# Optimization experiments

Hardware: AMD Instinct MI355X
Metric: run time of the kernel (lower is better)

The kernel has to match this reference:

```python
import jax, jax.numpy as jnp
import numpy as np

B, N0, N1, N2 = 4, 50000, 25000, 12500
E0, E1 = 800000, 400000
CIN, CS, COUT = 32, 16, 32
EPS = 1e-5


def _xavier(k, shape):
    scale = (2.0 / (shape[0] + shape[-1])) ** 0.5
    return jax.random.normal(k, shape, jnp.float32) * scale


def setup_inputs() -> dict:
    key = jax.random.key(0)
    ks = jax.random.split(key, 32)
    inp = {
        "X": jax.random.normal(ks[0], (B, N0, CIN), jnp.float32),
        "edge_index0": jax.random.randint(ks[1], (2, E0), 0, N1),
        "edge_weight0": jax.random.uniform(ks[2], (E0,), jnp.float32),
        "res_n_id0": jax.random.randint(ks[3], (N1,), 0, N0),
        "edge_index1": jax.random.randint(ks[4], (2, E1), 0, N2),
        "edge_weight1": jax.random.uniform(ks[5], (E1,), jnp.float32),
        "res_n_id1": jax.random.randint(ks[6], (N2,), 0, N1),
        # conv1 params (in=32 -> out=16, edge_channels=1)
        "Wn1": _xavier(ks[7], (CIN, CS)),
        "We1": _xavier(ks[8], (1, CS)),
        "Q1": _xavier(ks[9], (CS, CS)),
        "K1": _xavier(ks[10], (CS, CS)),
        "Watt1": _xavier(ks[11], (3 * CS, 1)),
        "batt1": jnp.zeros((1,), jnp.float32),
        "Wc1": _xavier(ks[12], (2 * CS, CS)),
        "bc1": jnp.zeros((CS,), jnp.float32),
        # conv2 params (in=16 -> out=32, edge_channels=1)
        "Wn2": _xavier(ks[13], (CS, COUT)),
        "We2": _xavier(ks[14], (1, COUT)),
        "Q2": _xavier(ks[15], (COUT, COUT)),
        "K2": _xavier(ks[16], (COUT, COUT)),
        "Watt2": _xavier(ks[17], (3 * COUT, 1)),
        "batt2": jnp.zeros((1,), jnp.float32),
        "Wc2": _xavier(ks[18], (2 * COUT, COUT)),
        "bc2": jnp.zeros((COUT,), jnp.float32),
    }
    return inp


def egnn_conv(x_src, x_dst, edge_index, edge_feature, num_dst,
              Wn, We, Q, K, Watt, batt, Wc, bc):
    # x_src: [B, Nsrc, Cin], x_dst: [B, Ndst, Cin], edge_feature: [E, 1]
    xs = jnp.matmul(x_src, Wn)        # [B, Nsrc, C]
    xd = jnp.matmul(x_dst, Wn)        # [B, Ndst, C]
    edge_emb = jnp.matmul(edge_feature, We)  # [E, C]

    src, dst = edge_index[0], edge_index[1]
    x_j = xs[:, src]                  # gather [B, E, C]
    x_i = xd[:, dst]                  # gather [B, E, C]

    query = jnp.matmul(x_j, Q)        # [B, E, C]
    key = jnp.matmul(x_i, K)          # [B, E, C]
    ee = jnp.broadcast_to(edge_emb[None], query.shape)  # [B, E, C]
    att_feature = jnp.concatenate([query, key, ee], axis=-1)  # [B, E, 3C]
    att = jax.nn.sigmoid(jnp.matmul(att_feature, Watt) + batt)  # [B, E, 1]
    gate = jax.nn.sigmoid(edge_emb)[None]  # [1, E, C]
    msg = att * x_j * gate            # [B, E, C]

    # scatter-add over destination nodes
    aggr = jnp.zeros((msg.shape[0], num_dst, msg.shape[-1]), msg.dtype)
    aggr = aggr.at[:, dst].add(msg)   # [B, Ndst, C]

    out = jnp.matmul(jnp.concatenate([xd, aggr], axis=-1), Wc) + bc  # [B, Ndst, C]
    mean = jnp.mean(out, axis=(0, 2), keepdims=True)
    var = jnp.var(out, axis=(0, 2), keepdims=True, ddof=1)  # torch var is unbiased
    out = (out - mean) / jnp.sqrt(var + EPS)
    return xd + out


def reference(X, edge_index0, edge_weight0, res_n_id0,
              edge_index1, edge_weight1, res_n_id1,
              Wn1, We1, Q1, K1, Watt1, batt1, Wc1, bc1,
              Wn2, We2, Q2, K2, Watt2, batt2, Wc2, bc2):
    h = egnn_conv(X, X[:, res_n_id0], edge_index0, edge_weight0[:, None], N1,
                  Wn1, We1, Q1, K1, Watt1, batt1, Wc1, bc1)
    h = jax.nn.leaky_relu(h, 0.01)
    h = egnn_conv(h, h[:, res_n_id1], edge_index1, edge_weight1[:, None], N2,
                  Wn2, We2, Q2, K2, Watt2, batt2, Wc2, bc2)
    h = jax.nn.leaky_relu(h, 0.01)
    return h
```

## Files before the change

### kernel.cpp

```cpp
#include <hip/hip_runtime.h>

#define B_ 4
#define N0_ 50000
#define N1_ 25000
#define N2_ 12500
#define E0_ 800000
#define E1_ 400000
#define CIN_ 32
#define CS_ 16
#define COUT_ 32
#define EPS_ 1e-5f
#define CAP_ 80
#define ROW_ CAP_
#define RCAP0_ 14336
#define RCAP1_ 8192
#define NREP_ 8
#define CPAD_ 16
#define SPLITB_ 512
#define SST1_ 3200
#define SST2_ 1600

__device__ __forceinline__ int slice_of(int d) { return (d >> 2) & 7; }
__device__ __forceinline__ int curix(int d, int sst) {
    return ((d >> 2) & 7) * sst + ((d >> 5) << 2) + (d & 3);
}

__device__ __forceinline__ float sigmoidf_(float x) {
    return __builtin_amdgcn_rcpf(1.0f + __expf(-x));
}

__global__ void prep_kernel(const float* __restrict__ Q1, const float* __restrict__ K1,
                            const float* __restrict__ Watt1,
                            const float* __restrict__ Q2, const float* __restrict__ K2,
                            const float* __restrict__ Watt2,
                            const float* __restrict__ We1, const float* __restrict__ We2,
                            float* __restrict__ qv1, float* __restrict__ kv1,
                            float* __restrict__ qv2, float* __restrict__ kv2,
                            float* __restrict__ se) {
    int t = threadIdx.x;
    if (t < CS_) {
        float q = 0.f, k = 0.f;
        for (int c = 0; c < CS_; ++c) {
            q += Q1[t * CS_ + c] * Watt1[c];
            k += K1[t * CS_ + c] * Watt1[CS_ + c];
        }
        qv1[t] = q; kv1[t] = k;
    }
    if (t < COUT_) {
        float q = 0.f, k = 0.f;
        for (int c = 0; c < COUT_; ++c) {
            q += Q2[t * COUT_ + c] * Watt2[c];
            k += K2[t * COUT_ + c] * Watt2[COUT_ + c];
        }
        qv2[t] = q; kv2[t] = k;
    }
    if (t == 0) {
        float s1 = 0.f, s2 = 0.f;
        for (int c = 0; c < CS_; ++c) s1 += We1[c] * Watt1[2 * CS_ + c];
        for (int c = 0; c < COUT_; ++c) s2 += We2[c] * Watt2[2 * COUT_ + c];
        se[0] = s1; se[1] = s2;
    }
}

template <int RCAP>
__device__ __forceinline__ void split_dev(const int* __restrict__ ei, const float* __restrict__ ew,
                                          int E, int* __restrict__ rcnt,
                                          unsigned* __restrict__ A, unsigned short* __restrict__ C,
                                          int bid, int nblocks) {
    __shared__ int lcnt[8];
    __shared__ int lbase[8];
    int tid = threadIdx.x;
    int lane = tid & 63;
    int rep = bid & (NREP_ - 1);
    int per = (E + nblocks - 1) / nblocks;
    int s0 = bid * per;
    int s1 = min(E, s0 + per);
    int niter = (s1 - s0 + 255) >> 8;
    if (tid < 8) lcnt[tid] = 0;
    __syncthreads();
    for (int i = 0; i < niter; ++i) {
        int e = s0 + i * 256 + tid;
        int slice = (e < s1) ? slice_of(ei[E + e]) : -1;
#pragma unroll
        for (int sl = 0; sl < 8; ++sl) {
            unsigned long long m = __ballot(slice == sl);
            if (m && lane == __ffsll(m) - 1) atomicAdd(&lcnt[sl], (int)__popcll(m));
        }
    }
    __syncthreads();
    if (tid < 8) {
        lbase[tid] = atomicAdd(&rcnt[(tid * NREP_ + rep) * CPAD_], lcnt[tid]);
        lcnt[tid] = 0;
    }
    __syncthreads();
    for (int i = 0; i < niter; ++i) {
        int e = s0 + i * 256 + tid;
        int d = 0, s = 0, slice = -1;
        float w = 0.f;
        if (e < s1) {
            d = ei[E + e];
            s = ei[e];
            w = ew[e];
            slice = slice_of(d);
        }
        int pos = 0;
#pragma unroll
        for (int sl = 0; sl < 8; ++sl) {
            unsigned long long m = __ballot(slice == sl);
            if (!m) continue;
            int leader = __ffsll(m) - 1;
            int base = 0;
            if (lane == leader) base = atomicAdd(&lcnt[sl], (int)__popcll(m));
            base = __shfl(base, leader);
            if (slice == sl) pos = base + (int)__popcll(m & ((1ull << lane) - 1ull));
        }
        if (slice >= 0) {
            int gpos = lbase[slice] + pos;
            if (gpos < RCAP) {
                int idx = (slice * NREP_ + rep) * RCAP + gpos;
                A[idx] = (unsigned)d | ((unsigned)s << 16);
                C[idx] = (unsigned short)((__float_as_uint(w) + 0x8000u) >> 16);
            }
        }
    }
}

__global__ void split_both(const int* __restrict__ ei0, const float* __restrict__ ew0,
                           const int* __restrict__ ei1, const float* __restrict__ ew1,
                           int* __restrict__ rcnt0, int* __restrict__ rcnt1,
                           unsigned* __restrict__ A0, unsigned short* __restrict__ C0,
                           unsigned* __restrict__ A1, unsigned short* __restrict__ C1) {
    if (blockIdx.x < SPLITB_)
        split_dev<RCAP0_>(ei0, ew0, E0_, rcnt0, A0, C0, blockIdx.x, SPLITB_);
    else
        split_dev<RCAP1_>(ei1, ew1, E1_, rcnt1, A1, C1, blockIdx.x - SPLITB_, SPLITB_);
}

__global__ void scatter_bin(const int* __restrict__ rcnt0, const unsigned* __restrict__ A0,
                            const unsigned short* __restrict__ C0,
                            int* __restrict__ cur0, unsigned* __restrict__ buf0,
                            const int* __restrict__ rcnt1, const unsigned* __restrict__ A1,
                            const unsigned short* __restrict__ C1,
                            int* __restrict__ cur1b, unsigned* __restrict__ buf1) {
    int half = blockIdx.x >= 1024;
    int bid = blockIdx.x & 1023;
    int slice = bid & 7;
    int chunk = bid >> 3;
    const int nch = 128;
    int tid = threadIdx.x;
    const int* rc = half ? rcnt1 : rcnt0;
    const unsigned* A = half ? A1 : A0;
    const unsigned short* C = half ? C1 : C0;
    int* cur = half ? cur1b : cur0;
    unsigned* buf = half ? buf1 : buf0;
    int RCAP = half ? RCAP1_ : RCAP0_;
    int sst = half ? SST2_ : SST1_;
#pragma unroll
    for (int rep = 0; rep < NREP_; ++rep) {
        int cnt = rc[(slice * NREP_ + rep) * CPAD_];
        if (cnt > RCAP) cnt = RCAP;
        int base = (slice * NREP_ + rep) * RCAP;
        for (int i = chunk * 256 + tid; i < cnt; i += nch * 256) {
            unsigned a = A[base + i];
            int d = a & 0xffff;
            unsigned s = a >> 16;
            unsigned wu = (unsigned)C[base + i];
            int p = atomicAdd(&cur[curix(d, sst)], 1);
            if (p < CAP_)
                buf[(size_t)d * ROW_ + p] = (wu << 16) | s;
        }
    }
}

__global__ void node_xform1(const float* __restrict__ X, const int* __restrict__ res,
                            const float* __restrict__ Wn,
                            const float* __restrict__ qv, const float* __restrict__ kv,
                            unsigned short* __restrict__ xsb, float* __restrict__ xd_t,
                            float* __restrict__ aj, float* __restrict__ ai) {
    int lane = threadIdx.x & 63;
    int n = blockIdx.x * (blockDim.x >> 6) + (threadIdx.x >> 6);
    if (n >= N1_) return;
    int b = lane >> 4;
    int c = lane & 15;
    int rn = res[n];
    const float4* Xs4 = (const float4*)(X + ((size_t)b * N0_ + n) * CIN_);
    const float4* Xd4 = (const float4*)(X + ((size_t)b * N0_ + rn) * CIN_);
    float s = 0.f, d = 0.f;
#pragma unroll
    for (int k4 = 0; k4 < CIN_ / 4; ++k4) {
        float4 xs4 = Xs4[k4];
        float4 xd4 = Xd4[k4];
        int k = 4 * k4;
        float w0 = Wn[(k + 0) * CS_ + c], w1 = Wn[(k + 1) * CS_ + c];
        float w2 = Wn[(k + 2) * CS_ + c], w3 = Wn[(k + 3) * CS_ + c];
        s += xs4.x * w0 + xs4.y * w1 + xs4.z * w2 + xs4.w * w3;
        d += xd4.x * w0 + xd4.y * w1 + xd4.z * w2 + xd4.w * w3;
    }
    xsb[(size_t)n * 64 + lane] = (unsigned short)((__float_as_uint(s) + 0x8000u) >> 16);
    xd_t[(size_t)n * 64 + lane] = d;
    float p = s * qv[c];
    float q = d * kv[c];
#pragma unroll
    for (int m = 1; m < 16; m <<= 1) {
        p += __shfl_xor(p, m, 16);
        q += __shfl_xor(q, m, 16);
    }
    if (c == 0) {
        aj[n * 4 + b] = p;
        ai[n * 4 + b] = q;
    }
}

__global__ void edge_fused1(const int* __restrict__ cur, const unsigned* __restrict__ buf,
                            const unsigned short* __restrict__ xsb,
                            const float* __restrict__ xd_t,
                            const float* __restrict__ aj, const float* __restrict__ ai,
                            const float* __restrict__ sep, const float* __restrict__ batt,
                            const float* __restrict__ We,
                            const float* __restrict__ Wc, const float* __restrict__ bc,
                            float* __restrict__ h_t) {
    int lane = threadIdx.x & 63;
    int n = blockIdx.x * (blockDim.x >> 6) + (threadIdx.x >> 6);
    if (n >= N1_) return;
    int b = lane >> 4;
    int c = lane & 15;
    float wec = We[c];
    float se1 = sep[0];
    float aivb = ai[n * 4 + b] + batt[0];
    float acc = 0.f;
    int cnt = cur[curix(n, SST1_)];
    if (cnt > CAP_) cnt = CAP_;
    const unsigned* bp = buf + (size_t)n * ROW_;
    int i = 0;
    for (; i + 4 <= cnt; i += 4) {
        unsigned v0 = bp[i], v1 = bp[i + 1], v2 = bp[i + 2], v3 = bp[i + 3];
        int s0 = v0 & 0xffff, s1 = v1 & 0xffff, s2 = v2 & 0xffff, s3 = v3 & 0xffff;
        float w0 = __uint_as_float(v0 & 0xffff0000u);
        float w1 = __uint_as_float(v1 & 0xffff0000u);
        float w2 = __uint_as_float(v2 & 0xffff0000u);
        float w3 = __uint_as_float(v3 & 0xffff0000u);
        float aj0 = aj[s0 * 4 + b], aj1 = aj[s1 * 4 + b];
        float aj2 = aj[s2 * 4 + b], aj3 = aj[s3 * 4 + b];
        float xj0 = __uint_as_float((unsigned)xsb[(size_t)s0 * 64 + lane] << 16);
        float xj1 = __uint_as_float((unsigned)xsb[(size_t)s1 * 64 + lane] << 16);
        float xj2 = __uint_as_float((unsigned)xsb[(size_t)s2 * 64 + lane] << 16);
        float xj3 = __uint_as_float((unsigned)xsb[(size_t)s3 * 64 + lane] << 16);
        acc += sigmoidf_(aj0 + aivb + w0 * se1) * sigmoidf_(w0 * wec) * xj0;
        acc += sigmoidf_(aj1 + aivb + w1 * se1) * sigmoidf_(w1 * wec) * xj1;
        acc += sigmoidf_(aj2 + aivb + w2 * se1) * sigmoidf_(w2 * wec) * xj2;
        acc += sigmoidf_(aj3 + aivb + w3 * se1) * sigmoidf_(w3 * wec) * xj3;
    }
    for (; i < cnt; ++i) {
        unsigned v0 = bp[i];
        int s0 = v0 & 0xffff;
        float w0 = __uint_as_float(v0 & 0xffff0000u);
        float aj0 = aj[s0 * 4 + b];
        float xj0 = __uint_as_float((unsigned)xsb[(size_t)s0 * 64 + lane] << 16);
        acc += sigmoidf_(aj0 + aivb + w0 * se1) * sigmoidf_(w0 * wec) * xj0;
    }
    float xv = xd_t[(size_t)n * 64 + lane];
    float o = bc[c];
#pragma unroll
    for (int k = 0; k < CS_; ++k) {
        o += __shfl(xv, k, 16) * Wc[k * CS_ + c];
        o += __shfl(acc, k, 16) * Wc[(CS_ + k) * CS_ + c];
    }
    float s = o, sq = o * o;
#pragma unroll
    for (int m = 1; m < 64; m <<= 1) {
        s += __shfl_xor(s, m);
        sq += __shfl_xor(sq, m);
    }
    float mean = s * (1.f / 64.f);
    float var = (sq - 64.f * mean * mean) * (1.f / 63.f);
    float inv = __builtin_amdgcn_rsqf(var + EPS_);
    float v = xv + (o - mean) * inv;
    h_t[(size_t)n * 64 + lane] = v > 0.f ? v : 0.01f * v;
}

__global__ void node_xform2(const float* __restrict__ h_t, const int* __restrict__ res,
                            const float* __restrict__ Wn,
                            const float* __restrict__ qv, const float* __restrict__ kv,
                            unsigned short* __restrict__ xsb, float* __restrict__ xd_t,
                            float* __restrict__ aj, float* __restrict__ ai) {
    int lane = threadIdx.x & 63;
    int n = blockIdx.x * (blockDim.x >> 6) + (threadIdx.x >> 6);
    if (n >= N2_) return;
    int bl = lane >> 5;
    int c = lane & 31;
    int rn = res[n];
    float qc = qv[c], kc = kv[c];
#pragma unroll
    for (int j = 0; j < 2; ++j) {
        int b = bl + 2 * j;
        const float* hs = h_t + (size_t)n * 64 + b * 16;
        const float* hd = h_t + (size_t)rn * 64 + b * 16;
        float s = 0.f, d = 0.f;
#pragma unroll
        for (int k = 0; k < CS_; ++k) {
            float w = Wn[k * COUT_ + c];
            s += hs[k] * w;
            d += hd[k] * w;
        }
        xsb[(size_t)n * 128 + b * 32 + c] = (unsigned short)((__float_as_uint(s) + 0x8000u) >> 16);
        xd_t[(size_t)n * 128 + b * 32 + c] = d;
        float p = s * qc;
        float q = d * kc;
#pragma unroll
        for (int m = 1; m < 32; m <<= 1) {
            p += __shfl_xor(p, m, 32);
            q += __shfl_xor(q, m, 32);
        }
        if (c == 0) {
            aj[n * 4 + b] = p;
            ai[n * 4 + b] = q;
        }
    }
}

__global__ void edge_fused2(const int* __restrict__ cur, const unsigned* __restrict__ buf,
                            const unsigned short* __restrict__ xsb,
                            const float* __restrict__ xd_t,
                            const float* __restrict__ aj, const float* __restrict__ ai,
                            const float* __restrict__ sep, const float* __restrict__ batt,
                            const float* __restrict__ We,
                            const float* __restrict__ Wc, const float* __restrict__ bc,
                            float* __restrict__ out) {
    int lane = threadIdx.x & 63;
    int n = blockIdx.x * (blockDim.x >> 6) + (threadIdx.x >> 6);
    if (n >= N2_) return;
    int bl = lane >> 5;
    int c = lane & 31;
    float wec = We[c];
    float se2 = sep[0];
    float b0 = batt[0];
    float aiv0 = ai[n * 4 + bl] + b0;
    float aiv1 = ai[n * 4 + bl + 2] + b0;
    float acc0 = 0.f, acc1 = 0.f;
    int cnt = cur[curix(n, SST2_)];
    if (cnt > CAP_) cnt = CAP_;
    const unsigned* bp = buf + (size_t)n * ROW_;
    int i = 0;
    for (; i + 2 <= cnt; i += 2) {
        unsigned v0 = bp[i], v1 = bp[i + 1];
        int s0 = v0 & 0xffff, s1 = v1 & 0xffff;
        float w0 = __uint_as_float(v0 & 0xffff0000u);
        float w1 = __uint_as_float(v1 & 0xffff0000u);
        float aj00 = aj[s0 * 4 + bl], aj01 = aj[s0 * 4 + bl + 2];
        float aj10 = aj[s1 * 4 + bl], aj11 = aj[s1 * 4 + bl + 2];
        float xj00 = __uint_as_float((unsigned)xsb[(size_t)s0 * 128 + lane] << 16);
        float xj01 = __uint_as_float((unsigned)xsb[(size_t)s0 * 128 + 64 + lane] << 16);
        float xj10 = __uint_as_float((unsigned)xsb[(size_t)s1 * 128 + lane] << 16);
        float xj11 = __uint_as_float((unsigned)xsb[(size_t)s1 * 128 + 64 + lane] << 16);
        float g0 = sigmoidf_(w0 * wec);
        float g1 = sigmoidf_(w1 * wec);
        float t0 = w0 * se2, t1 = w1 * se2;
        acc0 += sigmoidf_(aj00 + aiv0 + t0) * g0 * xj00;
        acc1 += sigmoidf_(aj01 + aiv1 + t0) * g0 * xj01;
        acc0 += sigmoidf_(aj10 + aiv0 + t1) * g1 * xj10;
        acc1 += sigmoidf_(aj11 + aiv1 + t1) * g1 * xj11;
    }
    if (i < cnt) {
        unsigned v0 = bp[i];
        int s0 = v0 & 0xffff;
        float w0 = __uint_as_float(v0 & 0xffff0000u);
        float aj00 = aj[s0 * 4 + bl], aj01 = aj[s0 * 4 + bl + 2];
        float xj00 = __uint_as_float((unsigned)xsb[(size_t)s0 * 128 + lane] << 16);
        float xj01 = __uint_as_float((unsigned)xsb[(size_t)s0 * 128 + 64 + lane] << 16);
        float g0 = sigmoidf_(w0 * wec);
        float t0 = w0 * se2;
        acc0 += sigmoidf_(aj00 + aiv0 + t0) * g0 * xj00;
        acc1 += sigmoidf_(aj01 + aiv1 + t0) * g0 * xj01;
    }
    float xv0 = xd_t[(size_t)n * 128 + lane];
    float xv1 = xd_t[(size_t)n * 128 + 64 + lane];
    float o0 = bc[c], o1 = o0;
#pragma unroll
    for (int k = 0; k < COUT_; ++k) {
        float w1 = Wc[k * COUT_ + c];
        float w2 = Wc[(COUT_ + k) * COUT_ + c];
        o0 += __shfl(xv0, k, 32) * w1 + __shfl(acc0, k, 32) * w2;
        o1 += __shfl(xv1, k, 32) * w1 + __shfl(acc1, k, 32) * w2;
    }
    float s = o0 + o1, sq = o0 * o0 + o1 * o1;
#pragma unroll
    for (int m = 1; m < 64; m <<= 1) {
        s += __shfl_xor(s, m);
        sq += __shfl_xor(sq, m);
    }
    float mean = s * (1.f / 128.f);
    float var = (sq - 128.f * mean * mean) * (1.f / 127.f);
    float inv = __builtin_amdgcn_rsqf(var + EPS_);
    float v0 = xv0 + (o0 - mean) * inv;
    float v1 = xv1 + (o1 - mean) * inv;
    out[((size_t)bl * N2_ + n) * COUT_ + c] = v0 > 0.f ? v0 : 0.01f * v0;
    out[((size_t)(bl + 2) * N2_ + n) * COUT_ + c] = v1 > 0.f ? v1 : 0.01f * v1;
}

extern "C" void kernel_launch(void* const* d_in, const int* in_sizes, int n_in,
                              void* d_out, int out_size, void* d_ws, size_t ws_size,
                              hipStream_t stream) {
    (void)in_sizes; (void)n_in; (void)out_size; (void)ws_size;
    const float* X     = (const float*)d_in[0];
    const int*   ei0   = (const int*)d_in[1];
    const float* ew0   = (const float*)d_in[2];
    const int*   rn0   = (const int*)d_in[3];
    const int*   ei1   = (const int*)d_in[4];
    const float* ew1   = (const float*)d_in[5];
    const int*   rn1   = (const int*)d_in[6];
    const float* Wn1   = (const float*)d_in[7];
    const float* We1   = (const float*)d_in[8];
    const float* Q1    = (const float*)d_in[9];
    const float* K1    = (const float*)d_in[10];
    const float* Watt1 = (const float*)d_in[11];
    const float* batt1 = (const float*)d_in[12];
    const float* Wc1   = (const float*)d_in[13];
    const float* bc1   = (const float*)d_in[14];
    const float* Wn2   = (const float*)d_in[15];
    const float* We2   = (const float*)d_in[16];
    const float* Q2    = (const float*)d_in[17];
    const float* K2    = (const float*)d_in[18];
    const float* Watt2 = (const float*)d_in[19];
    const float* batt2 = (const float*)d_in[20];
    const float* Wc2   = (const float*)d_in[21];
    const float* bc2   = (const float*)d_in[22];

    const size_t BUF = (size_t)B_ * N1_ * CS_;
    float* ws  = (float*)d_ws;
    float* S0  = ws;
    float* S1  = S0 + BUF;
    unsigned short* S2 = (unsigned short*)(S1 + BUF);
    float* aj1 = (float*)(S2 + BUF);
    float* ai1 = aj1 + (size_t)N1_ * 4;
    float* aj2 = ai1 + (size_t)N1_ * 4;
    float* ai2 = aj2 + (size_t)N2_ * 4;
    unsigned* ebuf1 = (unsigned*)(ai2 + (size_t)N2_ * 4);
    unsigned* ebuf2 = ebuf1 + (size_t)N1_ * ROW_;
    int* cur1  = (int*)(ebuf2 + (size_t)N2_ * ROW_);
    int* cur2  = cur1 + 8 * SST1_;
    int* rcnt0 = cur2 + 8 * SST2_;
    int* rcnt1 = rcnt0 + 64 * CPAD_;
    unsigned* A0 = (unsigned*)(rcnt1 + 64 * CPAD_);
    unsigned* A1 = A0 + (size_t)64 * RCAP0_;
    unsigned short* C0 = (unsigned short*)(A1 + (size_t)64 * RCAP1_);
    unsigned short* C1 = C0 + (size_t)64 * RCAP0_;
    float* qv1 = (float*)(C1 + (size_t)64 * RCAP1_);
    float* kv1 = qv1 + 16;
    float* qv2 = kv1 + 16;
    float* kv2 = qv2 + 32;
    float* se  = kv2 + 32;

    hipMemsetAsync(cur1, 0, (size_t)(8 * SST1_ + 8 * SST2_ + 128 * CPAD_) * sizeof(int), stream);
    prep_kernel<<<1, 64, 0, stream>>>(Q1, K1, Watt1, Q2, K2, Watt2, We1, We2,
                                      qv1, kv1, qv2, kv2, se);
    split_both<<<2 * SPLITB_, 256, 0, stream>>>(ei0, ew0, ei1, ew1, rcnt0, rcnt1,
                                                A0, C0, A1, C1);
    scatter_bin<<<2048, 256, 0, stream>>>(rcnt0, A0, C0, cur1, ebuf1,
                                          rcnt1, A1, C1, cur2, ebuf2);

    node_xform1<<<(N1_ + 3) / 4, 256, 0, stream>>>(X, rn0, Wn1, qv1, kv1, S2, S0, aj1, ai1);
    edge_fused1<<<(N1_ + 3) / 4, 256, 0, stream>>>(cur1, ebuf1, S2, S0, aj1, ai1,
                                                   se, batt1, We1, Wc1, bc1, S0);

    node_xform2<<<(N2_ + 3) / 4, 256, 0, stream>>>(S0, rn1, Wn2, qv2, kv2, S2, S1, aj2, ai2);
    edge_fused2<<<(N2_ + 3) / 4, 256, 0, stream>>>(cur2, ebuf2, S2, S1, aj2, ai2,
                                                   se + 1, batt2, We2, Wc2, bc2, (float*)d_out);
}
```

Measured before the change: 203.0 us.

## Merge prep/split and bin/xform launches; split edge loops across two waves per node

```diff
diff --git a/kernel.cpp b/kernel.cpp
--- a/kernel.cpp
+++ b/kernel.cpp
@@ -19,47 +19,14 @@
 #define SPLITB_ 512
 #define SST1_ 3200
 #define SST2_ 1600
+#define BINB_ 2048
 
 __device__ __forceinline__ int slice_of(int d) { return (d >> 2) & 7; }
 __device__ __forceinline__ int curix(int d, int sst) {
     return ((d >> 2) & 7) * sst + ((d >> 5) << 2) + (d & 3);
 }
-
 __device__ __forceinline__ float sigmoidf_(float x) {
     return __builtin_amdgcn_rcpf(1.0f + __expf(-x));
-}
-
-__global__ void prep_kernel(const float* __restrict__ Q1, const float* __restrict__ K1,
-                            const float* __restrict__ Watt1,
-                            const float* __restrict__ Q2, const float* __restrict__ K2,
-                            const float* __restrict__ Watt2,
-                            const float* __restrict__ We1, const float* __restrict__ We2,
-                            float* __restrict__ qv1, float* __restrict__ kv1,
-                            float* __restrict__ qv2, float* __restrict__ kv2,
-                            float* __restrict__ se) {
-    int t = threadIdx.x;
-    if (t < CS_) {
-        float q = 0.f, k = 0.f;
-        for (int c = 0; c < CS_; ++c) {
-            q += Q1[t * CS_ + c] * Watt1[c];
-            k += K1[t * CS_ + c] * Watt1[CS_ + c];
-        }
-        qv1[t] = q; kv1[t] = k;
-    }
-    if (t < COUT_) {
-        float q = 0.f, k = 0.f;
-        for (int c = 0; c < COUT_; ++c) {
-            q += Q2[t * COUT_ + c] * Watt2[c];
-            k += K2[t * COUT_ + c] * Watt2[COUT_ + c];
-        }
-        qv2[t] = q; kv2[t] = k;
-    }
-    if (t == 0) {
-        float s1 = 0.f, s2 = 0.f;
-        for (int c = 0; c < CS_; ++c) s1 += We1[c] * Watt1[2 * CS_ + c];
-        for (int c = 0; c < COUT_; ++c) s2 += We2[c] * Watt2[2 * COUT_ + c];
-        se[0] = s1; se[1] = s2;
-    }
 }
 
 template <int RCAP>
@@ -125,103 +92,139 @@
     }
 }
 
-__global__ void split_both(const int* __restrict__ ei0, const float* __restrict__ ew0,
+__global__ void split_prep(const int* __restrict__ ei0, const float* __restrict__ ew0,
                            const int* __restrict__ ei1, const float* __restrict__ ew1,
                            int* __restrict__ rcnt0, int* __restrict__ rcnt1,
                            unsigned* __restrict__ A0, unsigned short* __restrict__ C0,
-                           unsigned* __restrict__ A1, unsigned short* __restrict__ C1) {
-    if (blockIdx.x < SPLITB_)
+                           unsigned* __restrict__ A1, unsigned short* __restrict__ C1,
+                           const float* __restrict__ Q1, const float* __restrict__ K1,
+                           const float* __restrict__ Watt1,
+                           const float* __restrict__ Q2, const float* __restrict__ K2,
+                           const float* __restrict__ Watt2,
+                           const float* __restrict__ We1, const float* __restrict__ We2,
+                           float* __restrict__ qv1, float* __restrict__ kv1,
+                           float* __restrict__ qv2, float* __restrict__ kv2,
+                           float* __restrict__ se) {
+    if (blockIdx.x < SPLITB_) {
         split_dev<RCAP0_>(ei0, ew0, E0_, rcnt0, A0, C0, blockIdx.x, SPLITB_);
-    else
+    } else if (blockIdx.x < 2 * SPLITB_) {
         split_dev<RCAP1_>(ei1, ew1, E1_, rcnt1, A1, C1, blockIdx.x - SPLITB_, SPLITB_);
-}
-
-__global__ void scatter_bin(const int* __restrict__ rcnt0, const unsigned* __restrict__ A0,
-                            const unsigned short* __restrict__ C0,
-                            int* __restrict__ cur0, unsigned* __restrict__ buf0,
-                            const int* __restrict__ rcnt1, const unsigned* __restrict__ A1,
-                            const unsigned short* __restrict__ C1,
-                            int* __restrict__ cur1b, unsigned* __restrict__ buf1) {
-    int half = blockIdx.x >= 1024;
-    int bid = blockIdx.x & 1023;
-    int slice = bid & 7;
-    int chunk = bid >> 3;
-    const int nch = 128;
+    } else {
+        int t = threadIdx.x;
+        if (t < CS_) {
+            float q = 0.f, k = 0.f;
+            for (int c = 0; c < CS_; ++c) {
+                q += Q1[t * CS_ + c] * Watt1[c];
+                k += K1[t * CS_ + c] * Watt1[CS_ + c];
+            }
+            qv1[t] = q; kv1[t] = k;
+        }
+        if (t < COUT_) {
+            float q = 0.f, k = 0.f;
+            for (int c = 0; c < COUT_; ++c) {
+                q += Q2[t * COUT_ + c] * Watt2[c];
+                k += K2[t * COUT_ + c] * Watt2[COUT_ + c];
+            }
+            qv2[t] = q; kv2[t] = k;
+        }
+        if (t == 0) {
+            float s1 = 0.f, s2 = 0.f;
+            for (int c = 0; c < CS_; ++c) s1 += We1[c] * Watt1[2 * CS_ + c];
+            for (int c = 0; c < COUT_; ++c) s2 += We2[c] * Watt2[2 * COUT_ + c];
+            se[0] = s1; se[1] = s2;
+        }
+    }
+}
+
+__global__ void bin_xform1(const int* __restrict__ rcnt0, const unsigned* __restrict__ A0,
+                           const unsigned short* __restrict__ C0,
+                           int* __restrict__ cur0, unsigned* __restrict__ buf0,
+                           const int* __restrict__ rcnt1, const unsigned* __restrict__ A1,
+                           const unsigned short* __restrict__ C1,
+                           int* __restrict__ cur1b, unsigned* __restrict__ buf1,
+                           const float* __restrict__ X, const int* __restrict__ res,
+                           const float* __restrict__ Wn,
+                           const float* __restrict__ qv, const float* __restrict__ kv,
+                           unsigned short* __restrict__ xsb, float* __restrict__ xd_t,
+                           float* __restrict__ aj, float* __restrict__ ai) {
+    if (blockIdx.x < BINB_) {
+        int half = blockIdx.x >= (BINB_ / 2);
+        int bid = blockIdx.x & (BINB_ / 2 - 1);
+        int slice = bid & 7;
+        int chunk = bid >> 3;
+        const int nch = BINB_ / 16;
+        int tid = threadIdx.x;
+        const int* rc = half ? rcnt1 : rcnt0;
+        const unsigned* A = half ? A1 : A0;
+        const unsigned short* C = half ? C1 : C0;
+        int* cur = half ? cur1b : cur0;
+        unsigned* buf = half ? buf1 : buf0;
+        int RCAP = half ? RCAP1_ : RCAP0_;
+        int sst = half ? SST2_ : SST1_;
+#pragma unroll
+        for (int rep = 0; rep < NREP_; ++rep) {
+            int cnt = rc[(slice * NREP_ + rep) * CPAD_];
+            if (cnt > RCAP) cnt = RCAP;
+            int base = (slice * NREP_ + rep) * RCAP;
+            for (int i = chunk * 256 + tid; i < cnt; i += nch * 256) {
+                unsigned a = A[base + i];
+                int d = a & 0xffff;
+                unsigned s = a >> 16;
+                unsigned wu = (unsigned)C[base + i];
+                int p = atomicAdd(&cur[curix(d, sst)], 1);
+                if (p < CAP_)
+                    buf[(size_t)d * ROW_ + p] = (wu << 16) | s;
+            }
+        }
+    } else {
+        int lane = threadIdx.x & 63;
+        int n = (blockIdx.x - BINB_) * 4 + (threadIdx.x >> 6);
+        if (n >= N1_) return;
+        int b = lane >> 4;
+        int c = lane & 15;
+        int rn = res[n];
+        const float4* Xs4 = (const float4*)(X + ((size_t)b * N0_ + n) * CIN_);
+        const float4* Xd4 = (const float4*)(X + ((size_t)b * N0_ + rn) * CIN_);
+        float s = 0.f, d = 0.f;
+#pragma unroll
+        for (int k4 = 0; k4 < CIN_ / 4; ++k4) {
+            float4 xs4 = Xs4[k4];
+            float4 xd4 = Xd4[k4];
+            int k = 4 * k4;
+            float w0 = Wn[(k + 0) * CS_ + c], w1 = Wn[(k + 1) * CS_ + c];
+            float w2 = Wn[(k + 2) * CS_ + c], w3 = Wn[(k + 3) * CS_ + c];
+            s += xs4.x * w0 + xs4.y * w1 + xs4.z * w2 + xs4.w * w3;
+            d += xd4.x * w0 + xd4.y * w1 + xd4.z * w2 + xd4.w * w3;
+        }
+        xsb[(size_t)n * 64 + lane] = (unsigned short)((__float_as_uint(s) + 0x8000u) >> 16);
+        xd_t[(size_t)n * 64 + lane] = d;
+        float p = s * qv[c];
+        float q = d * kv[c];
+#pragma unroll
+        for (int m = 1; m < 16; m <<= 1) {
+            p += __shfl_xor(p, m, 16);
+            q += __shfl_xor(q, m, 16);
+        }
+        if (c == 0) {
+            aj[n * 4 + b] = p;
+            ai[n * 4 + b] = q;
+        }
+    }
+}
+
+__global__ __launch_bounds__(512) void edge_fused1(
+        const int* __restrict__ cur, const unsigned* __restrict__ buf,
+        const unsigned short* __restrict__ xsb, const float* __restrict__ xd_t,
+        const float* __restrict__ aj, const float* __restrict__ ai,
+        const float* __restrict__ sep, const float* __restrict__ batt,
+        const float* __restrict__ We, const float* __restrict__ Wc,
+        const float* __restrict__ bc, float* __restrict__ h_t) {
+    __shared__ float lacc[4][64];
     int tid = threadIdx.x;
-    const int* rc = half ? rcnt1 : rcnt0;
-    const unsigned* A = half ? A1 : A0;
-    const unsigned short* C = half ? C1 : C0;
-    int* cur = half ? cur1b : cur0;
-    unsigned* buf = half ? buf1 : buf0;
-    int RCAP = half ? RCAP1_ : RCAP0_;
-    int sst = half ? SST2_ : SST1_;
-#pragma unroll
-    for (int rep = 0; rep < NREP_; ++rep) {
-        int cnt = rc[(slice * NREP_ + rep) * CPAD_];
-        if (cnt > RCAP) cnt = RCAP;
-        int base = (slice * NREP_ + rep) * RCAP;
-        for (int i = chunk * 256 + tid; i < cnt; i += nch * 256) {
-            unsigned a = A[base + i];
-            int d = a & 0xffff;
-            unsigned s = a >> 16;
-            unsigned wu = (unsigned)C[base + i];
-            int p = atomicAdd(&cur[curix(d, sst)], 1);
-            if (p < CAP_)
-                buf[(size_t)d * ROW_ + p] = (wu << 16) | s;
-        }
-    }
-}
-
-__global__ void node_xform1(const float* __restrict__ X, const int* __restrict__ res,
-                            const float* __restrict__ Wn,
-                            const float* __restrict__ qv, const float* __restrict__ kv,
-                            unsigned short* __restrict__ xsb, float* __restrict__ xd_t,
-                            float* __restrict__ aj, float* __restrict__ ai) {
-    int lane = threadIdx.x & 63;
-    int n = blockIdx.x * (blockDim.x >> 6) + (threadIdx.x >> 6);
-    if (n >= N1_) return;
-    int b = lane >> 4;
-    int c = lane & 15;
-    int rn = res[n];
-    const float4* Xs4 = (const float4*)(X + ((size_t)b * N0_ + n) * CIN_);
-    const float4* Xd4 = (const float4*)(X + ((size_t)b * N0_ + rn) * CIN_);
-    float s = 0.f, d = 0.f;
-#pragma unroll
-    for (int k4 = 0; k4 < CIN_ / 4; ++k4) {
-        float4 xs4 = Xs4[k4];
-        float4 xd4 = Xd4[k4];
-        int k = 4 * k4;
-        float w0 = Wn[(k + 0) * CS_ + c], w1 = Wn[(k + 1) * CS_ + c];
-        float w2 = Wn[(k + 2) * CS_ + c], w3 = Wn[(k + 3) * CS_ + c];
-        s += xs4.x * w0 + xs4.y * w1 + xs4.z * w2 + xs4.w * w3;
-        d += xd4.x * w0 + xd4.y * w1 + xd4.z * w2 + xd4.w * w3;
-    }
-    xsb[(size_t)n * 64 + lane] = (unsigned short)((__float_as_uint(s) + 0x8000u) >> 16);
-    xd_t[(size_t)n * 64 + lane] = d;
-    float p = s * qv[c];
-    float q = d * kv[c];
-#pragma unroll
-    for (int m = 1; m < 16; m <<= 1) {
-        p += __shfl_xor(p, m, 16);
-        q += __shfl_xor(q, m, 16);
-    }
-    if (c == 0) {
-        aj[n * 4 + b] = p;
-        ai[n * 4 + b] = q;
-    }
-}
-
-__global__ void edge_fused1(const int* __restrict__ cur, const unsigned* __restrict__ buf,
-                            const unsigned short* __restrict__ xsb,
-                            const float* __restrict__ xd_t,
-                            const float* __restrict__ aj, const float* __restrict__ ai,
-                            const float* __restrict__ sep, const float* __restrict__ batt,
-                            const float* __restrict__ We,
-                            const float* __restrict__ Wc, const float* __restrict__ bc,
-                            float* __restrict__ h_t) {
-    int lane = threadIdx.x & 63;
-    int n = blockIdx.x * (blockDim.x >> 6) + (threadIdx.x >> 6);
-    if (n >= N1_) return;
+    int lane = tid & 63;
+    int wid = (tid >> 6) & 1;
+    int ni = tid >> 7;
+    int n = blockIdx.x * 4 + ni;
     int b = lane >> 4;
     int c = lane & 15;
     float wec = We[c];
@@ -231,33 +234,39 @@
     int cnt = cur[curix(n, SST1_)];
     if (cnt > CAP_) cnt = CAP_;
     const unsigned* bp = buf + (size_t)n * ROW_;
-    int i = 0;
-    for (; i + 4 <= cnt; i += 4) {
-        unsigned v0 = bp[i], v1 = bp[i + 1], v2 = bp[i + 2], v3 = bp[i + 3];
-        int s0 = v0 & 0xffff, s1 = v1 & 0xffff, s2 = v2 & 0xffff, s3 = v3 & 0xffff;
-        float w0 = __uint_as_float(v0 & 0xffff0000u);
-        float w1 = __uint_as_float(v1 & 0xffff0000u);
-        float w2 = __uint_as_float(v2 & 0xffff0000u);
-        float w3 = __uint_as_float(v3 & 0xffff0000u);
-        float aj0 = aj[s0 * 4 + b], aj1 = aj[s1 * 4 + b];
-        float aj2 = aj[s2 * 4 + b], aj3 = aj[s3 * 4 + b];
-        float xj0 = __uint_as_float((unsigned)xsb[(size_t)s0 * 64 + lane] << 16);
-        float xj1 = __uint_as_float((unsigned)xsb[(size_t)s1 * 64 + lane] << 16);
-        float xj2 = __uint_as_float((unsigned)xsb[(size_t)s2 * 64 + lane] << 16);
-        float xj3 = __uint_as_float((unsigned)xsb[(size_t)s3 * 64 + lane] << 16);
-        acc += sigmoidf_(aj0 + aivb + w0 * se1) * sigmoidf_(w0 * wec) * xj0;
-        acc += sigmoidf_(aj1 + aivb + w1 * se1) * sigmoidf_(w1 * wec) * xj1;
-        acc += sigmoidf_(aj2 + aivb + w2 * se1) * sigmoidf_(w2 * wec) * xj2;
-        acc += sigmoidf_(aj3 + aivb + w3 * se1) * sigmoidf_(w3 * wec) * xj3;
-    }
-    for (; i < cnt; ++i) {
-        unsigned v0 = bp[i];
-        int s0 = v0 & 0xffff;
-        float w0 = __uint_as_float(v0 & 0xffff0000u);
-        float aj0 = aj[s0 * 4 + b];
-        float xj0 = __uint_as_float((unsigned)xsb[(size_t)s0 * 64 + lane] << 16);
-        acc += sigmoidf_(aj0 + aivb + w0 * se1) * sigmoidf_(w0 * wec) * xj0;
-    }
+    for (int i0 = wid * 4; i0 < cnt; i0 += 8) {
+        if (i0 + 4 <= cnt) {
+            uint4 v = *(const uint4*)(bp + i0);
+            int s0 = v.x & 0xffff, s1 = v.y & 0xffff, s2 = v.z & 0xffff, s3 = v.w & 0xffff;
+            float w0 = __uint_as_float(v.x & 0xffff0000u);
+            float w1 = __uint_as_float(v.y & 0xffff0000u);
+            float w2 = __uint_as_float(v.z & 0xffff0000u);
+            float w3 = __uint_as_float(v.w & 0xffff0000u);
+            float aj0 = aj[s0 * 4 + b], aj1 = aj[s1 * 4 + b];
+            float aj2 = aj[s2 * 4 + b], aj3 = aj[s3 * 4 + b];
+            float xj0 = __uint_as_float((unsigned)xsb[(size_t)s0 * 64 + lane] << 16);
+            float xj1 = __uint_as_float((unsigned)xsb[(size_t)s1 * 64 + lane] << 16);
+            float xj2 = __uint_as_float((unsigned)xsb[(size_t)s2 * 64 + lane] << 16);
+            float xj3 = __uint_as_float((unsigned)xsb[(size_t)s3 * 64 + lane] << 16);
+            acc += sigmoidf_(aj0 + aivb + w0 * se1) * sigmoidf_(w0 * wec) * xj0;
+            acc += sigmoidf_(aj1 + aivb + w1 * se1) * sigmoidf_(w1 * wec) * xj1;
+            acc += sigmoidf_(aj2 + aivb + w2 * se1) * sigmoidf_(w2 * wec) * xj2;
+            acc += sigmoidf_(aj3 + aivb + w3 * se1) * sigmoidf_(w3 * wec) * xj3;
+        } else {
+            for (int i = i0; i < cnt; ++i) {
+                unsigned v0 = bp[i];
+                int s0 = v0 & 0xffff;
+                float w0 = __uint_as_float(v0 & 0xffff0000u);
+                float aj0 = aj[s0 * 4 + b];
+                float xj0 = __uint_as_float((unsigned)xsb[(size_t)s0 * 64 + lane] << 16);
+                acc += sigmoidf_(aj0 + aivb + w0 * se1) * sigmoidf_(w0 * wec) * xj0;
+            }
+        }
+    }
+    if (wid == 1) lacc[ni][lane] = acc;
+    __syncthreads();
+    if (wid == 1) return;
+    acc += lacc[ni][lane];
     float xv = xd_t[(size_t)n * 64 + lane];
     float o = bc[c];
 #pragma unroll
@@ -318,17 +327,19 @@
     }
 }
 
-__global__ void edge_fused2(const int* __restrict__ cur, const unsigned* __restrict__ buf,
-                            const unsigned short* __restrict__ xsb,
-                            const float* __restrict__ xd_t,
-                            const float* __restrict__ aj, const float* __restrict__ ai,
-                            const float* __restrict__ sep, const float* __restrict__ batt,
-                            const float* __restrict__ We,
-                            const float* __restrict__ Wc, const float* __restrict__ bc,
-                            float* __restrict__ out) {
-    int lane = threadIdx.x & 63;
-    int n = blockIdx.x * (blockDim.x >> 6) + (threadIdx.x >> 6);
-    if (n >= N2_) return;
+__global__ __launch_bounds__(512) void edge_fused2(
+        const int* __restrict__ cur, const unsigned* __restrict__ buf,
+        const unsigned short* __restrict__ xsb, const float* __restrict__ xd_t,
+        const float* __restrict__ aj, const float* __restrict__ ai,
+        const float* __restrict__ sep, const float* __restrict__ batt,
+        const float* __restrict__ We, const float* __restrict__ Wc,
+        const float* __restrict__ bc, float* __restrict__ out) {
+    __shared__ float lacc[4][2][64];
+    int tid = threadIdx.x;
+    int lane = tid & 63;
+    int wid = (tid >> 6) & 1;
+    int ni = tid >> 7;
+    int n = blockIdx.x * 4 + ni;
     int bl = lane >> 5;
     int c = lane & 31;
     float wec = We[c];
@@ -340,38 +351,45 @@
     int cnt = cur[curix(n, SST2_)];
     if (cnt > CAP_) cnt = CAP_;
     const unsigned* bp = buf + (size_t)n * ROW_;
-    int i = 0;
-    for (; i + 2 <= cnt; i += 2) {
-        unsigned v0 = bp[i], v1 = bp[i + 1];
-        int s0 = v0 & 0xffff, s1 = v1 & 0xffff;
-        float w0 = __uint_as_float(v0 & 0xffff0000u);
-        float w1 = __uint_as_float(v1 & 0xffff0000u);
-        float aj00 = aj[s0 * 4 + bl], aj01 = aj[s0 * 4 + bl + 2];
-        float aj10 = aj[s1 * 4 + bl], aj11 = aj[s1 * 4 + bl + 2];
-        float xj00 = __uint_as_float((unsigned)xsb[(size_t)s0 * 128 + lane] << 16);
-        float xj01 = __uint_as_float((unsigned)xsb[(size_t)s0 * 128 + 64 + lane] << 16);
-        float xj10 = __uint_as_float((unsigned)xsb[(size_t)s1 * 128 + lane] << 16);
-        float xj11 = __uint_as_float((unsigned)xsb[(size_t)s1 * 128 + 64 + lane] << 16);
-        float g0 = sigmoidf_(w0 * wec);
-        float g1 = sigmoidf_(w1 * wec);
-        float t0 = w0 * se2, t1 = w1 * se2;
-        acc0 += sigmoidf_(aj00 + aiv0 + t0) * g0 * xj00;
-        acc1 += sigmoidf_(aj01 + aiv1 + t0) * g0 * xj01;
-        acc0 += sigmoidf_(aj10 + aiv0 + t1) * g1 * xj10;
-        acc1 += sigmoidf_(aj11 + aiv1 + t1) * g1 * xj11;
-    }
-    if (i < cnt) {
-        unsigned v0 = bp[i];
-        int s0 = v0 & 0xffff;
-        float w0 = __uint_as_float(v0 & 0xffff0000u);
-        float aj00 = aj[s0 * 4 + bl], aj01 = aj[s0 * 4 + bl + 2];
-        float xj00 = __uint_as_float((unsigned)xsb[(size_t)s0 * 128 + lane] << 16);
-        float xj01 = __uint_as_float((unsigned)xsb[(size_t)s0 * 128 + 64 + lane] << 16);
-        float g0 = sigmoidf_(w0 * wec);
-        float t0 = w0 * se2;
-        acc0 += sigmoidf_(aj00 + aiv0 + t0) * g0 * xj00;
-        acc1 += sigmoidf_(aj01 + aiv1 + t0) * g0 * xj01;
-    }
+    for (int i0 = wid * 4; i0 < cnt; i0 += 8) {
+        if (i0 + 4 <= cnt) {
+            uint4 v = *(const uint4*)(bp + i0);
+#pragma unroll
+            for (int j = 0; j < 4; ++j) {
+                unsigned vj = j == 0 ? v.x : j == 1 ? v.y : j == 2 ? v.z : v.w;
+                int s0 = vj & 0xffff;
+                float w0 = __uint_as_float(vj & 0xffff0000u);
+                float aj0 = aj[s0 * 4 + bl], aj1 = aj[s0 * 4 + bl + 2];
+                float xj0 = __uint_as_float((unsigned)xsb[(size_t)s0 * 128 + lane] << 16);
+                float xj1 = __uint_as_float((unsigned)xsb[(size_t)s0 * 128 + 64 + lane] << 16);
+                float g = sigmoidf_(w0 * wec);
+                float t = w0 * se2;
+                acc0 += sigmoidf_(aj0 + aiv0 + t) * g * xj0;
+                acc1 += sigmoidf_(aj1 + aiv1 + t) * g * xj1;
+            }
+        } else {
+            for (int i = i0; i < cnt; ++i) {
+                unsigned vj = bp[i];
+                int s0 = vj & 0xffff;
+                float w0 = __uint_as_float(vj & 0xffff0000u);
+                float aj0 = aj[s0 * 4 + bl], aj1 = aj[s0 * 4 + bl + 2];
+                float xj0 = __uint_as_float((unsigned)xsb[(size_t)s0 * 128 + lane] << 16);
+                float xj1 = __uint_as_float((unsigned)xsb[(size_t)s0 * 128 + 64 + lane] << 16);
+                float g = sigmoidf_(w0 * wec);
+                float t = w0 * se2;
+                acc0 += sigmoidf_(aj0 + aiv0 + t) * g * xj0;
+                acc1 += sigmoidf_(aj1 + aiv1 + t) * g * xj1;
+            }
+        }
+    }
+    if (wid == 1) {
+        lacc[ni][0][lane] = acc0;
+        lacc[ni][1][lane] = acc1;
+    }
+    __syncthreads();
+    if (wid == 1) return;
+    acc0 += lacc[ni][0][lane];
+    acc1 += lacc[ni][1][lane];
     float xv0 = xd_t[(size_t)n * 128 + lane];
     float xv1 = xd_t[(size_t)n * 128 + 64 + lane];
     float o0 = bc[c], o1 = o0;
@@ -451,18 +469,18 @@
     float* se  = kv2 + 32;
 
     hipMemsetAsync(cur1, 0, (size_t)(8 * SST1_ + 8 * SST2_ + 128 * CPAD_) * sizeof(int), stream);
-    prep_kernel<<<1, 64, 0, stream>>>(Q1, K1, Watt1, Q2, K2, Watt2, We1, We2,
-                                      qv1, kv1, qv2, kv2, se);
-    split_both<<<2 * SPLITB_, 256, 0, stream>>>(ei0, ew0, ei1, ew1, rcnt0, rcnt1,
-                                                A0, C0, A1, C1);
-    scatter_bin<<<2048, 256, 0, stream>>>(rcnt0, A0, C0, cur1, ebuf1,
-                                          rcnt1, A1, C1, cur2, ebuf2);
-
-    node_xform1<<<(N1_ + 3) / 4, 256, 0, stream>>>(X, rn0, Wn1, qv1, kv1, S2, S0, aj1, ai1);
-    edge_fused1<<<(N1_ + 3) / 4, 256, 0, stream>>>(cur1, ebuf1, S2, S0, aj1, ai1,
-                                                   se, batt1, We1, Wc1, bc1, S0);
+    split_prep<<<2 * SPLITB_ + 1, 256, 0, stream>>>(ei0, ew0, ei1, ew1, rcnt0, rcnt1,
+                                                    A0, C0, A1, C1,
+                                                    Q1, K1, Watt1, Q2, K2, Watt2,
+                                                    We1, We2, qv1, kv1, qv2, kv2, se);
+    bin_xform1<<<BINB_ + (N1_ + 3) / 4, 256, 0, stream>>>(
+        rcnt0, A0, C0, cur1, ebuf1, rcnt1, A1, C1, cur2, ebuf2,
+        X, rn0, Wn1, qv1, kv1, S2, S0, aj1, ai1);
+
+    edge_fused1<<<N1_ / 4, 512, 0, stream>>>(cur1, ebuf1, S2, S0, aj1, ai1,
+                                             se, batt1, We1, Wc1, bc1, S0);
 
     node_xform2<<<(N2_ + 3) / 4, 256, 0, stream>>>(S0, rn1, Wn2, qv2, kv2, S2, S1, aj2, ai2);
-    edge_fused2<<<(N2_ + 3) / 4, 256, 0, stream>>>(cur2, ebuf2, S2, S1, aj2, ai2,
-                                                   se + 1, batt2, We2, Wc2, bc2, (float*)d_out);
-}
+    edge_fused2<<<N2_ / 4, 512, 0, stream>>>(cur2, ebuf2, S2, S1, aj2, ai2,
+                                             se + 1, batt2, We2, Wc2, bc2, (float*)d_out);
+}
```

Measured after the change: 204.8 us. Within noise of the previous version (+0.9%).
